# Optimization experiments

Hardware: AMD Instinct MI355X
Metric: run time of the kernel (lower is better)

The kernel has to match this reference:

```python
import jax, jax.numpy as jnp
import numpy as np

K = 7          # kernel_size
PAD = 3        # padding
GROUPS = 8
OUTC = 128
INC = 128
REFINE = True


def conv1x1(x, w):
    # x: [B,C,H,W], w: [O,C] (1x1 conv, no bias)
    return jnp.einsum('oc,bchw->bohw', w, x)


def unfold2d(x, k):
    # x: [B,C,Hp,Wp] -> [B,C,h,w,k,k], stride 1 (matches torch unfold(2,k).unfold(3,k))
    B, C, Hp, Wp = x.shape
    h, w = Hp - k + 1, Wp - k + 1
    patches = jnp.stack([x[:, :, i:i + h, j:j + w] for i in range(k) for j in range(k)], axis=-1)
    return patches.reshape(B, C, h, w, k, k)


def unfold1d(x, k, axis):
    # sliding window of size k, stride 1, along axis 2 (rows) or 3 (cols)
    if axis == 2:
        h = x.shape[2] - k + 1
        return jnp.stack([x[:, :, i:i + h, :] for i in range(k)], axis=-1)  # [B,C,h,W,k]
    else:
        w = x.shape[3] - k + 1
        return jnp.stack([x[:, :, :, j:j + w] for j in range(k)], axis=-1)  # [B,C,H,w,k]


def _forward(feature_map, wq, wk, wv, rel_h, rel_w):
    c = feature_map.shape[1] // 2
    fm_t0, fm_t1 = feature_map[:, :c], feature_map[:, c:]
    B, _, H, W = fm_t0.shape
    cg = OUTC // GROUPS

    padded_t0 = jnp.pad(fm_t0, ((0, 0), (0, 0), (PAD, PAD), (PAD, PAD)))
    q = conv1x1(fm_t1, wq)                 # [B,OUTC,H,W]
    k_full = conv1x1(padded_t0, wk)        # [B,OUTC,H+2p,W+2p]
    v_full = conv1x1(padded_t0, wv)

    k_win = unfold2d(k_full, K)            # [B,OUTC,H,W,K,K]
    k_h, k_w = k_win[:, :OUTC // 2], k_win[:, OUTC // 2:]
    k_win = jnp.concatenate([k_h + rel_h, k_w + rel_w], axis=1)
    k_win = k_win.reshape(B, GROUPS, cg, H, W, K * K)
    v_win = unfold2d(v_full, K).reshape(B, GROUPS, cg, H, W, K * K)

    qg = q.reshape(B, GROUPS, cg, H, W, 1)
    attn = jax.nn.softmax(jnp.sum(qg * k_win, axis=2), axis=-1)  # [B,G,H,W,K*K]
    out = jnp.einsum('bnhwk,bnchwk->bnchw', attn, v_win).reshape(B, OUTC, H, W)

    if REFINE:
        win = 2 * K + 1
        p_col = jnp.pad(fm_t0, ((0, 0), (0, 0), (K, K), (0, 0)))
        p_row = jnp.pad(fm_t0, ((0, 0), (0, 0), (0, 0), (K, K)))
        k_col = unfold1d(conv1x1(p_col, wk), win, 2).reshape(B, GROUPS, cg, H, W, win)
        k_row = unfold1d(conv1x1(p_row, wk), win, 3).reshape(B, GROUPS, cg, H, W, win)
        v_col = unfold1d(conv1x1(p_col, wv), win, 2).reshape(B, GROUPS, cg, H, W, win)
        v_row = unfold1d(conv1x1(p_row, wv), win, 3).reshape(B, GROUPS, cg, H, W, win)

        a_row = jax.nn.softmax(jnp.sum(qg * k_row, axis=2), axis=-1)
        a_col = jax.nn.softmax(jnp.sum(qg * k_col, axis=2), axis=-1)
        out = out + jnp.einsum('bnhwk,bnchwk->bnchw', a_row, v_row).reshape(B, OUTC, H, W)
        out = out + jnp.einsum('bnhwk,bnchwk->bnchw', a_col, v_col).reshape(B, OUTC, H, W)
    return out


def setup_inputs() -> dict:
    key = jax.random.key(0)
    ks = jax.random.split(key, 6)
    B, H, W = 2, 64, 64
    feature_map = jax.random.normal(ks[0], (B, 2 * INC, H, W), dtype=jnp.float32)
    # kaiming_normal fan_out for 1x1 conv: std = sqrt(2 / outc)
    std = float(np.sqrt(2.0 / OUTC))
    wq = jax.random.normal(ks[1], (OUTC, INC), dtype=jnp.float32) * std
    wk = jax.random.normal(ks[2], (OUTC, INC), dtype=jnp.float32) * std
    wv = jax.random.normal(ks[3], (OUTC, INC), dtype=jnp.float32) * std
    rel_h = jax.random.normal(ks[4], (OUTC // 2, 1, 1, K, 1), dtype=jnp.float32)
    rel_w = jax.random.normal(ks[5], (OUTC // 2, 1, 1, 1, K), dtype=jnp.float32)
    return {"feature_map": feature_map, "wq": wq, "wk": wk, "wv": wv,
            "rel_h": rel_h, "rel_w": rel_w}


def reference(feature_map, wq, wk, wv, rel_h, rel_w):
    return _forward(feature_map, wq, wk, wv, rel_h, rel_w)
```

## Files before the change

kernel.cpp:

```cpp
#include <hip/hip_runtime.h>
#include <hip/hip_bf16.h>

__device__ __forceinline__ float bf2f(unsigned short u) {
    union { unsigned int i; float f; } v; v.i = ((unsigned int)u) << 16; return v.f;
}
__device__ __forceinline__ unsigned short f2bf(float f) {
    __hip_bfloat16 h = __float2bfloat16(f);
    return *reinterpret_cast<unsigned short*>(&h);
}


#define CANVAS_SLAB 102400

__global__ __launch_bounds__(256) void pad_zero_kernel(uint4* __restrict__ p)
{
    const size_t i = (size_t)blockIdx.x * 256 + threadIdx.x;
    p[i] = make_uint4(0u, 0u, 0u, 0u);
}

__global__ __launch_bounds__(256) void conv_kernel(
    const float* __restrict__ fm,
    const float* __restrict__ wq, const float* __restrict__ wk,
    const float* __restrict__ wv,
    float* __restrict__ Qout,
    unsigned short* __restrict__ K0,
    unsigned short* __restrict__ V0)
{
    const int sel = blockIdx.z;
    const int by  = blockIdx.y;
    const float* W = (sel == 0) ? wq : ((sel == 1) ? wk : wv);
    const int c0 = (sel == 0) ? 128 : 0;

    __shared__ float w_s[64 * 68];
    __shared__ float x_s[64 * 68];

    const int tid = threadIdx.x;
    const int P0  = blockIdx.x * 64;
    const int b   = P0 >> 12;
    const int hw0 = P0 & 4095;

    float acc[4][4];
    #pragma unroll
    for (int i = 0; i < 4; ++i)
        #pragma unroll
        for (int j = 0; j < 4; ++j) acc[i][j] = 0.f;

    const int ocb = (tid >> 4) * 4;
    const int pxb = (tid & 15) * 4;

    for (int kh = 0; kh < 128; kh += 64) {
        {
            const int o    = tid >> 2;
            const int koff = (tid & 3) * 16;
            #pragma unroll
            for (int i = 0; i < 4; ++i) {
                float4 v = *(const float4*)(W + (size_t)(by * 64 + o) * 128 + kh + koff + i * 4);
                w_s[(koff + i * 4 + 0) * 68 + o] = v.x;
                w_s[(koff + i * 4 + 1) * 68 + o] = v.y;
                w_s[(koff + i * 4 + 2) * 68 + o] = v.z;
                w_s[(koff + i * 4 + 3) * 68 + o] = v.w;
            }
        }
        {
            const int c  = tid >> 2;
            const int pc = (tid & 3) * 16;
            const float* src = fm + (((size_t)(b * 256 + c0 + kh + c)) << 12) + hw0 + pc;
            #pragma unroll
            for (int i = 0; i < 4; ++i)
                *(float4*)(&x_s[c * 68 + pc + i * 4]) = *(const float4*)(src + i * 4);
        }
        __syncthreads();
        #pragma unroll 8
        for (int k = 0; k < 64; ++k) {
            float4 wa = *(const float4*)(&w_s[k * 68 + ocb]);
            float4 xv = *(const float4*)(&x_s[k * 68 + pxb]);
            const float wf[4] = {wa.x, wa.y, wa.z, wa.w};
            const float xf[4] = {xv.x, xv.y, xv.z, xv.w};
            #pragma unroll
            for (int i = 0; i < 4; ++i)
                #pragma unroll
                for (int j = 0; j < 4; ++j) acc[i][j] += wf[i] * xf[j];
        }
        __syncthreads();
    }

    const int oc  = by * 64 + ocb;
    const int g   = oc >> 4;
    const int lci = oc & 15;
    const int hh  = hw0 >> 6;
    #pragma unroll
    for (int pj = 0; pj < 4; ++pj) {
        const int ww = pxb + pj;
        if (sel == 0) {
            const size_t base = ((((size_t)(b * 8 + g)) << 12) + (hh * 64 + ww)) * 16 + lci;
            *(float4*)(Qout + base) = make_float4(acc[0][pj], acc[1][pj], acc[2][pj], acc[3][pj]);
        } else {
            const size_t cbase = (size_t)(b * 8 + g) * CANVAS_SLAB
                               + ((size_t)((hh + 8) * 80 + (ww + 8))) * 16 + lci;
            unsigned short tmp[4];
            #pragma unroll
            for (int i = 0; i < 4; ++i) tmp[i] = f2bf(acc[i][pj]);
            unsigned short* dst = ((sel == 1) ? K0 : V0) + cbase;
            *(uint2*)dst = *(const uint2*)tmp;
        }
    }
}

struct KV16 { uint4 a, b; };
__device__ __forceinline__ KV16 ld16(const unsigned short* p) {
    KV16 r; r.a = *(const uint4*)p; r.b = *(const uint4*)(p + 8); return r;
}
__device__ __forceinline__ float dotq(const float* q, const KV16& k) {
    const unsigned short* u = (const unsigned short*)&k;
    float s = 0.f;
    #pragma unroll
    for (int c = 0; c < 16; ++c) s += q[c] * bf2f(u[c]);
    return s;
}
__device__ __forceinline__ void axpyq(float* acc, float wgt, const KV16& v) {
    const unsigned short* u = (const unsigned short*)&v;
    #pragma unroll
    for (int c = 0; c < 16; ++c) acc[c] += wgt * bf2f(u[c]);
}

__global__ __launch_bounds__(256) void attn_kernel(
    const float* __restrict__ Q,
    const unsigned short* __restrict__ K0,
    const unsigned short* __restrict__ V0,
    const float* __restrict__ rel_h,
    const float* __restrict__ rel_w,
    float* __restrict__ P)
{
    const int tid  = threadIdx.x;
    const int w    = tid & 63;
    const int h    = blockIdx.x * 4 + (tid >> 6);
    const int g    = blockIdx.y;
    const int b    = blockIdx.z / 3;
    const int part = blockIdx.z % 3;

    const size_t slabQ = ((size_t)(b * 8 + g)) << 16;
    const float* qptr = Q + slabQ + (size_t)(h * 64 + w) * 16;

    float qr[16];
    #pragma unroll
    for (int ci = 0; ci < 16; ++ci) qr[ci] = qptr[ci];

    const unsigned short* Kp = K0 + (size_t)(b * 8 + g) * CANVAS_SLAB;
    const unsigned short* Vp = V0 + (size_t)(b * 8 + g) * CANVAS_SLAB;

    #define CIDX(y, x) (((size_t)(((y) + 8) * 80 + ((x) + 8))) << 4)

    float acc[16];
    #pragma unroll
    for (int ci = 0; ci < 16; ++ci) acc[ci] = 0.f;

    if (part == 0) {
        float qrel[7];
        const float* rel = (g < 4) ? (rel_h + g * 112) : (rel_w + (g - 4) * 112);
        #pragma unroll
        for (int t = 0; t < 7; ++t) {
            float s = 0.f;
            #pragma unroll
            for (int ci = 0; ci < 16; ++ci) s += qr[ci] * rel[ci * 7 + t];
            qrel[t] = s;
        }
        const bool bias_i = (g < 4);
        float sc[49];
        float mx = -3.4e38f;
        #pragma unroll
        for (int i = 0; i < 7; ++i) {
            const int y = h + i - 3;
            #pragma unroll
            for (int j = 0; j < 7; ++j) {
                const int x = w + j - 3;
                float d = dotq(qr, ld16(Kp + CIDX(y, x)));
                d += bias_i ? qrel[i] : qrel[j];
                sc[i * 7 + j] = d;
                mx = fmaxf(mx, d);
            }
        }
        float den = 0.f;
        #pragma unroll
        for (int k = 0; k < 49; ++k) { sc[k] = __expf(sc[k] - mx); den += sc[k]; }
        const float inv = 1.f / den;
        #pragma unroll
        for (int i = 0; i < 7; ++i) {
            const int y = h + i - 3;
            #pragma unroll
            for (int j = 0; j < 7; ++j) {
                const int x = w + j - 3;
                axpyq(acc, sc[i * 7 + j] * inv, ld16(Vp + CIDX(y, x)));
            }
        }
    } else if (part == 1) {
        float sc[15];
        float mx = -3.4e38f;
        #pragma unroll
        for (int j = 0; j < 15; ++j) {
            const int x = w + j - 7;
            const float d = dotq(qr, ld16(Kp + CIDX(h, x)));
            sc[j] = d; mx = fmaxf(mx, d);
        }
        float den = 0.f;
        #pragma unroll
        for (int j = 0; j < 15; ++j) { sc[j] = __expf(sc[j] - mx); den += sc[j]; }
        const float inv = 1.f / den;
        #pragma unroll
        for (int j = 0; j < 15; ++j) {
            const int x = w + j - 7;
            axpyq(acc, sc[j] * inv, ld16(Vp + CIDX(h, x)));
        }
    } else {
        float sc[15];
        float mx = -3.4e38f;
        #pragma unroll
        for (int i = 0; i < 15; ++i) {
            const int y = h + i - 7;
            const float d = dotq(qr, ld16(Kp + CIDX(y, w)));
            sc[i] = d; mx = fmaxf(mx, d);
        }
        float den = 0.f;
        #pragma unroll
        for (int i = 0; i < 15; ++i) { sc[i] = __expf(sc[i] - mx); den += sc[i]; }
        const float inv = 1.f / den;
        #pragma unroll
        for (int i = 0; i < 15; ++i) {
            const int y = h + i - 7;
            axpyq(acc, sc[i] * inv, ld16(Vp + CIDX(y, w)));
        }
    }
    #undef CIDX

    float* op = P + ((((size_t)part * 2 + b) * 128 + g * 16) << 12) + h * 64 + w;
    #pragma unroll
    for (int ci = 0; ci < 16; ++ci)
        op[(size_t)ci << 12] = acc[ci];
}

__global__ __launch_bounds__(256) void combine_kernel(
    const float4* __restrict__ P, float4* __restrict__ out)
{
    const size_t i = (size_t)blockIdx.x * 256 + threadIdx.x;
    const float4 a = P[i];
    const float4 c = P[i + 262144];
    const float4 d = P[i + 524288];
    out[i] = make_float4(a.x + c.x + d.x, a.y + c.y + d.y,
                         a.z + c.z + d.z, a.w + c.w + d.w);
}

extern "C" void kernel_launch(void* const* d_in, const int* in_sizes, int n_in,
                              void* d_out, int out_size, void* d_ws, size_t ws_size,
                              hipStream_t stream) {
    (void)in_sizes; (void)n_in; (void)ws_size; (void)out_size;
    const float* fm    = (const float*)d_in[0];
    const float* wq    = (const float*)d_in[1];
    const float* wk    = (const float*)d_in[2];
    const float* wv    = (const float*)d_in[3];
    const float* rel_h = (const float*)d_in[4];
    const float* rel_w = (const float*)d_in[5];

    float* Q = (float*)d_ws;
    unsigned short* K0 = (unsigned short*)(Q + 1048576);
    unsigned short* V0 = K0 + 16 * CANVAS_SLAB;
    float* P = (float*)(V0 + 16 * CANVAS_SLAB);

    pad_zero_kernel<<<dim3(1600), dim3(256), 0, stream>>>((uint4*)K0);

    conv_kernel<<<dim3(128, 2, 3), dim3(256), 0, stream>>>(
        fm, wq, wk, wv, Q, K0, V0);
    attn_kernel<<<dim3(16, 8, 6), dim3(256), 0, stream>>>(
        Q, K0, V0, rel_h, rel_w, P);
    combine_kernel<<<dim3(1024), dim3(256), 0, stream>>>(
        (const float4*)P, (float4*)d_out);
}
```

Before: 109.1 us.

## Split 7x7 window softmax into three row chunks merged flash-style in combine

```diff
diff --git a/kernel.cpp b/kernel.cpp
--- a/kernel.cpp
+++ b/kernel.cpp
@@ -123,20 +123,70 @@
     for (int c = 0; c < 16; ++c) acc[c] += wgt * bf2f(u[c]);
 }
 
+#define CIDX(y, x) (((size_t)(((y) + 8) * 80 + ((x) + 8))) << 4)
+
+template<int I0, int NI>
+__device__ __forceinline__ void main_chunk(
+    const float* qr, const unsigned short* Kp, const unsigned short* Vp,
+    const float* __restrict__ rel_h, const float* __restrict__ rel_w,
+    int g, int h, int w, float* acc, float& mx, float& den)
+{
+    float qrel[7];
+    const float* rel = (g < 4) ? (rel_h + g * 112) : (rel_w + (g - 4) * 112);
+    #pragma unroll
+    for (int t = 0; t < 7; ++t) {
+        float s = 0.f;
+        #pragma unroll
+        for (int ci = 0; ci < 16; ++ci) s += qr[ci] * rel[ci * 7 + t];
+        qrel[t] = s;
+    }
+    const bool bias_i = (g < 4);
+
+    float sc[NI * 7];
+    mx = -3.4e38f;
+    #pragma unroll
+    for (int i = 0; i < NI; ++i) {
+        const int y = h + (I0 + i) - 3;
+        #pragma unroll
+        for (int j = 0; j < 7; ++j) {
+            const int x = w + j - 3;
+            float d = dotq(qr, ld16(Kp + CIDX(y, x)));
+            d += bias_i ? qrel[I0 + i] : qrel[j];
+            sc[i * 7 + j] = d;
+            mx = fmaxf(mx, d);
+        }
+    }
+    den = 0.f;
+    #pragma unroll
+    for (int k = 0; k < NI * 7; ++k) { sc[k] = __expf(sc[k] - mx); den += sc[k]; }
+    #pragma unroll
+    for (int i = 0; i < NI; ++i) {
+        const int y = h + (I0 + i) - 3;
+        #pragma unroll
+        for (int j = 0; j < 7; ++j) {
+            const int x = w + j - 3;
+            axpyq(acc, sc[i * 7 + j], ld16(Vp + CIDX(y, x)));
+        }
+    }
+}
+
 __global__ __launch_bounds__(256) void attn_kernel(
     const float* __restrict__ Q,
     const unsigned short* __restrict__ K0,
     const unsigned short* __restrict__ V0,
     const float* __restrict__ rel_h,
     const float* __restrict__ rel_w,
-    float* __restrict__ P)
-{
-    const int tid  = threadIdx.x;
-    const int w    = tid & 63;
-    const int h    = blockIdx.x * 4 + (tid >> 6);
-    const int g    = blockIdx.y;
-    const int b    = blockIdx.z / 3;
-    const int part = blockIdx.z % 3;
+    float* __restrict__ ACC,
+    float* __restrict__ Mb,
+    float* __restrict__ Db)
+{
+    const int tid = threadIdx.x;
+    const int w   = tid & 63;
+    const int h   = blockIdx.x * 4 + (tid >> 6);
+    const int g   = blockIdx.y;
+    const int z   = blockIdx.z;
+    const int pz  = z >> 1;
+    const int b   = z & 1;
 
     const size_t slabQ = ((size_t)(b * 8 + g)) << 16;
     const float* qptr = Q + slabQ + (size_t)(h * 64 + w) * 16;
@@ -148,104 +198,109 @@
     const unsigned short* Kp = K0 + (size_t)(b * 8 + g) * CANVAS_SLAB;
     const unsigned short* Vp = V0 + (size_t)(b * 8 + g) * CANVAS_SLAB;
 
-    #define CIDX(y, x) (((size_t)(((y) + 8) * 80 + ((x) + 8))) << 4)
-
     float acc[16];
     #pragma unroll
     for (int ci = 0; ci < 16; ++ci) acc[ci] = 0.f;
-
-    if (part == 0) {
-        float qrel[7];
-        const float* rel = (g < 4) ? (rel_h + g * 112) : (rel_w + (g - 4) * 112);
-        #pragma unroll
-        for (int t = 0; t < 7; ++t) {
-            float s = 0.f;
-            #pragma unroll
-            for (int ci = 0; ci < 16; ++ci) s += qr[ci] * rel[ci * 7 + t];
-            qrel[t] = s;
-        }
-        const bool bias_i = (g < 4);
-        float sc[49];
-        float mx = -3.4e38f;
-        #pragma unroll
-        for (int i = 0; i < 7; ++i) {
-            const int y = h + i - 3;
-            #pragma unroll
-            for (int j = 0; j < 7; ++j) {
-                const int x = w + j - 3;
-                float d = dotq(qr, ld16(Kp + CIDX(y, x)));
-                d += bias_i ? qrel[i] : qrel[j];
-                sc[i * 7 + j] = d;
-                mx = fmaxf(mx, d);
-            }
-        }
-        float den = 0.f;
-        #pragma unroll
-        for (int k = 0; k < 49; ++k) { sc[k] = __expf(sc[k] - mx); den += sc[k]; }
-        const float inv = 1.f / den;
-        #pragma unroll
-        for (int i = 0; i < 7; ++i) {
-            const int y = h + i - 3;
-            #pragma unroll
-            for (int j = 0; j < 7; ++j) {
-                const int x = w + j - 3;
-                axpyq(acc, sc[i * 7 + j] * inv, ld16(Vp + CIDX(y, x)));
-            }
-        }
-    } else if (part == 1) {
+    float mx, den;
+
+    if (pz == 0) {
+        main_chunk<4, 3>(qr, Kp, Vp, rel_h, rel_w, g, h, w, acc, mx, den);
+    } else if (pz == 1) {
+        main_chunk<0, 2>(qr, Kp, Vp, rel_h, rel_w, g, h, w, acc, mx, den);
+    } else if (pz == 2) {
+        main_chunk<2, 2>(qr, Kp, Vp, rel_h, rel_w, g, h, w, acc, mx, den);
+    } else if (pz == 3) {
         float sc[15];
-        float mx = -3.4e38f;
+        mx = -3.4e38f;
         #pragma unroll
         for (int j = 0; j < 15; ++j) {
             const int x = w + j - 7;
             const float d = dotq(qr, ld16(Kp + CIDX(h, x)));
             sc[j] = d; mx = fmaxf(mx, d);
         }
-        float den = 0.f;
+        den = 0.f;
         #pragma unroll
         for (int j = 0; j < 15; ++j) { sc[j] = __expf(sc[j] - mx); den += sc[j]; }
-        const float inv = 1.f / den;
         #pragma unroll
         for (int j = 0; j < 15; ++j) {
             const int x = w + j - 7;
-            axpyq(acc, sc[j] * inv, ld16(Vp + CIDX(h, x)));
+            axpyq(acc, sc[j], ld16(Vp + CIDX(h, x)));
         }
     } else {
         float sc[15];
-        float mx = -3.4e38f;
+        mx = -3.4e38f;
         #pragma unroll
         for (int i = 0; i < 15; ++i) {
             const int y = h + i - 7;
             const float d = dotq(qr, ld16(Kp + CIDX(y, w)));
             sc[i] = d; mx = fmaxf(mx, d);
         }
-        float den = 0.f;
+        den = 0.f;
         #pragma unroll
         for (int i = 0; i < 15; ++i) { sc[i] = __expf(sc[i] - mx); den += sc[i]; }
-        const float inv = 1.f / den;
         #pragma unroll
         for (int i = 0; i < 15; ++i) {
             const int y = h + i - 7;
-            axpyq(acc, sc[i] * inv, ld16(Vp + CIDX(y, w)));
-        }
-    }
-    #undef CIDX
-
-    float* op = P + ((((size_t)part * 2 + b) * 128 + g * 16) << 12) + h * 64 + w;
+            axpyq(acc, sc[i], ld16(Vp + CIDX(y, w)));
+        }
+    }
+
+    const int hw = h * 64 + w;
+    float* op = ACC + ((((size_t)(pz * 2 + b)) * 128 + g * 16) << 12) + hw;
     #pragma unroll
     for (int ci = 0; ci < 16; ++ci)
         op[(size_t)ci << 12] = acc[ci];
-}
+    const size_t md = ((((size_t)(pz * 2 + b)) * 8 + g) << 12) + hw;
+    Mb[md] = mx;
+    Db[md] = den;
+}
+#undef CIDX
 
 __global__ __launch_bounds__(256) void combine_kernel(
-    const float4* __restrict__ P, float4* __restrict__ out)
-{
-    const size_t i = (size_t)blockIdx.x * 256 + threadIdx.x;
-    const float4 a = P[i];
-    const float4 c = P[i + 262144];
-    const float4 d = P[i + 524288];
-    out[i] = make_float4(a.x + c.x + d.x, a.y + c.y + d.y,
-                         a.z + c.z + d.z, a.w + c.w + d.w);
+    const float4* __restrict__ ACC,
+    const float* __restrict__ Mb, const float* __restrict__ Db,
+    float4* __restrict__ out)
+{
+    const int idx = blockIdx.x * 256 + threadIdx.x;
+    const int i4  = idx & 1023;
+    const int ch  = (idx >> 10) & 127;
+    const int b   = idx >> 17;
+    const int g   = ch >> 4;
+
+    const float4* M4 = (const float4*)Mb;
+    const float4* D4 = (const float4*)Db;
+
+    float4 A[5], Mv[3], Dv[5];
+    #pragma unroll
+    for (int p = 0; p < 5; ++p) {
+        A[p]  = ACC[(((size_t)(p * 2 + b) * 128 + ch) << 10) + i4];
+        Dv[p] = D4[(((size_t)(p * 2 + b) * 8 + g) << 10) + i4];
+    }
+    #pragma unroll
+    for (int p = 0; p < 3; ++p)
+        Mv[p] = M4[(((size_t)(p * 2 + b) * 8 + g) << 10) + i4];
+
+    const float* a0 = (const float*)&A[0]; const float* a1 = (const float*)&A[1];
+    const float* a2 = (const float*)&A[2]; const float* a3 = (const float*)&A[3];
+    const float* a4 = (const float*)&A[4];
+    const float* m0 = (const float*)&Mv[0]; const float* m1 = (const float*)&Mv[1];
+    const float* m2 = (const float*)&Mv[2];
+    const float* d0 = (const float*)&Dv[0]; const float* d1 = (const float*)&Dv[1];
+    const float* d2 = (const float*)&Dv[2]; const float* d3 = (const float*)&Dv[3];
+    const float* d4 = (const float*)&Dv[4];
+
+    float res[4];
+    #pragma unroll
+    for (int c = 0; c < 4; ++c) {
+        const float M  = fmaxf(m0[c], fmaxf(m1[c], m2[c]));
+        const float e0 = __expf(m0[c] - M);
+        const float e1 = __expf(m1[c] - M);
+        const float e2 = __expf(m2[c] - M);
+        const float num = a0[c] * e0 + a1[c] * e1 + a2[c] * e2;
+        const float den = d0[c] * e0 + d1[c] * e1 + d2[c] * e2;
+        res[c] = num / den + a3[c] / d3[c] + a4[c] / d4[c];
+    }
+    out[idx] = make_float4(res[0], res[1], res[2], res[3]);
 }
 
 extern "C" void kernel_launch(void* const* d_in, const int* in_sizes, int n_in,
@@ -262,14 +317,16 @@
     float* Q = (float*)d_ws;
     unsigned short* K0 = (unsigned short*)(Q + 1048576);
     unsigned short* V0 = K0 + 16 * CANVAS_SLAB;
-    float* P = (float*)(V0 + 16 * CANVAS_SLAB);
+    float* ACC = (float*)(V0 + 16 * CANVAS_SLAB);
+    float* Mb  = ACC + 5242880;
+    float* Db  = Mb + 327680;
 
     pad_zero_kernel<<<dim3(1600), dim3(256), 0, stream>>>((uint4*)K0);
 
     conv_kernel<<<dim3(128, 2, 3), dim3(256), 0, stream>>>(
         fm, wq, wk, wv, Q, K0, V0);
-    attn_kernel<<<dim3(16, 8, 6), dim3(256), 0, stream>>>(
-        Q, K0, V0, rel_h, rel_w, P);
+    attn_kernel<<<dim3(16, 8, 10), dim3(256), 0, stream>>>(
+        Q, K0, V0, rel_h, rel_w, ACC, Mb, Db);
     combine_kernel<<<dim3(1024), dim3(256), 0, stream>>>(
-        (const float4*)P, (float4*)d_out);
-}
+        (const float4*)ACC, Mb, Db, (float4*)d_out);
+}
```

Measured after the change: 105.0 us, median of 2. -3.7%, faster.
